# Optimization experiments

Measured on AMD Instinct MI355X. Metric: run time of the kernel, lower is better.

The kernel has to match this reference:

```python
import jax, jax.numpy as jnp
import numpy as np

ROWS = 1048576
DIM = 64
N_CHUNKS = 32
B = 32768


def setup_inputs() -> dict:
    key = jax.random.key(0)
    k_t, k_w, k_i0, k_i1 = jax.random.split(key, 4)
    bound = DIM ** (-0.5)
    table = jax.random.uniform(k_t, (ROWS, DIM), jnp.float32, -bound, bound)
    weights = jax.random.uniform(k_w, (ROWS * DIM, 1), jnp.float32, -1.0, 1.0)
    # Precomputed PolyHash outputs (fixed non-learned universal hashes)
    idx0 = jax.random.randint(k_i0, (B, N_CHUNKS), 0, ROWS, dtype=jnp.int64 if jax.config.jax_enable_x64 else jnp.int32)
    idx1 = jax.random.randint(k_i1, (B, N_CHUNKS), 0, ROWS * DIM, dtype=jnp.int64 if jax.config.jax_enable_x64 else jnp.int32)
    return {"table": table, "weights": weights, "idx0": idx0, "idx1": idx1}


def reference(table, weights, idx0, idx1):
    # vecs: [B, n_chunks, dim]; w: [B, n_chunks, 1]
    vecs = table[idx0]
    w = weights[idx1]
    return jnp.mean(vecs * w, axis=1)  # [B, dim]
```

## Files before the change

### kernel.cpp

```cpp
#include <hip/hip_runtime.h>

#define N_B 32768
#define N_CHUNKS 32
#define DIM 64

__global__ __launch_bounds__(256) void WeightedHashEmbedding_kernel(
    const float* __restrict__ table,
    const float* __restrict__ weights,
    const int*   __restrict__ idx0,
    const int*   __restrict__ idx1,
    float*       __restrict__ out)
{
    const int tid  = threadIdx.x;
    const int b    = blockIdx.x * 16 + (tid >> 4);
    const int quad = tid & 15;

    const int4* p0 = (const int4*)(idx0 + b * N_CHUNKS);
    const int4* p1 = (const int4*)(idx1 + b * N_CHUNKS);

    float4 acc = make_float4(0.f, 0.f, 0.f, 0.f);

    #pragma unroll 2
    for (int g = 0; g < N_CHUNKS / 4; ++g) {
        const int4 r0 = p0[g];
        const int4 r1 = p1[g];

        const float w0 = weights[r1.x];
        const float w1 = weights[r1.y];
        const float w2 = weights[r1.z];
        const float w3 = weights[r1.w];

        const float4 v0 = ((const float4*)(table + (size_t)r0.x * DIM))[quad];
        const float4 v1 = ((const float4*)(table + (size_t)r0.y * DIM))[quad];
        const float4 v2 = ((const float4*)(table + (size_t)r0.z * DIM))[quad];
        const float4 v3 = ((const float4*)(table + (size_t)r0.w * DIM))[quad];

        acc.x += v0.x * w0; acc.y += v0.y * w0; acc.z += v0.z * w0; acc.w += v0.w * w0;
        acc.x += v1.x * w1; acc.y += v1.y * w1; acc.z += v1.z * w1; acc.w += v1.w * w1;
        acc.x += v2.x * w2; acc.y += v2.y * w2; acc.z += v2.z * w2; acc.w += v2.w * w2;
        acc.x += v3.x * w3; acc.y += v3.y * w3; acc.z += v3.z * w3; acc.w += v3.w * w3;
    }

    const float inv = 1.0f / (float)N_CHUNKS;
    float4 r;
    r.x = acc.x * inv; r.y = acc.y * inv; r.z = acc.z * inv; r.w = acc.w * inv;
    ((float4*)(out + (size_t)b * DIM))[quad] = r;
}

extern "C" void kernel_launch(void* const* d_in, const int* in_sizes, int n_in,
                              void* d_out, int out_size, void* d_ws, size_t ws_size,
                              hipStream_t stream) {
    const float* table   = (const float*)d_in[0];
    const float* weights = (const float*)d_in[1];
    const int*   idx0    = (const int*)d_in[2];
    const int*   idx1    = (const int*)d_in[3];
    float*       out     = (float*)d_out;

    const int rows_per_block = 16;
    const int grid = N_B / rows_per_block;

    WeightedHashEmbedding_kernel<<<grid, 256, 0, stream>>>(table, weights, idx0, idx1, out);
}
```

Before: 473.4 us.

## Map one wavefront per batch row with lane-broadcast indices and weights

Each 64-lane wavefront now handles one batch row, with each lane owning one output dimension. The 32 indices and the 32 gathered weights are loaded once per wave, one per lane, and broadcast with readlane instead of being re-read by every thread. All 32 table-row loads are issued up front before any accumulation, which exposes more memory-level parallelism. The trade-offs are scalar 4-byte loads per lane instead of float4 loads, and higher register use to hold the 32 values in flight.

```diff
diff --git a/kernel.cpp b/kernel.cpp
--- a/kernel.cpp
+++ b/kernel.cpp
@@ -11,40 +11,30 @@
     const int*   __restrict__ idx1,
     float*       __restrict__ out)
 {
-    const int tid  = threadIdx.x;
-    const int b    = blockIdx.x * 16 + (tid >> 4);
-    const int quad = tid & 15;
+    const int lane = threadIdx.x & 63;
+    const int wid  = threadIdx.x >> 6;
+    const int b    = blockIdx.x * 4 + wid;
 
-    const int4* p0 = (const int4*)(idx0 + b * N_CHUNKS);
-    const int4* p1 = (const int4*)(idx1 + b * N_CHUNKS);
+    const int c  = lane & 31;
+    const int i0 = idx0[b * N_CHUNKS + c];
+    const int i1 = idx1[b * N_CHUNKS + c];
+    const float wv = weights[i1];
 
-    float4 acc = make_float4(0.f, 0.f, 0.f, 0.f);
-
-    #pragma unroll 2
-    for (int g = 0; g < N_CHUNKS / 4; ++g) {
-        const int4 r0 = p0[g];
-        const int4 r1 = p1[g];
-
-        const float w0 = weights[r1.x];
-        const float w1 = weights[r1.y];
-        const float w2 = weights[r1.z];
-        const float w3 = weights[r1.w];
-
-        const float4 v0 = ((const float4*)(table + (size_t)r0.x * DIM))[quad];
-        const float4 v1 = ((const float4*)(table + (size_t)r0.y * DIM))[quad];
-        const float4 v2 = ((const float4*)(table + (size_t)r0.z * DIM))[quad];
-        const float4 v3 = ((const float4*)(table + (size_t)r0.w * DIM))[quad];
-
-        acc.x += v0.x * w0; acc.y += v0.y * w0; acc.z += v0.z * w0; acc.w += v0.w * w0;
-        acc.x += v1.x * w1; acc.y += v1.y * w1; acc.z += v1.z * w1; acc.w += v1.w * w1;
-        acc.x += v2.x * w2; acc.y += v2.y * w2; acc.z += v2.z * w2; acc.w += v2.w * w2;
-        acc.x += v3.x * w3; acc.y += v3.y * w3; acc.z += v3.z * w3; acc.w += v3.w * w3;
+    float v[N_CHUNKS];
+    #pragma unroll
+    for (int cc = 0; cc < N_CHUNKS; ++cc) {
+        const int row = __builtin_amdgcn_readlane(i0, cc);
+        v[cc] = table[(size_t)row * DIM + lane];
     }
 
-    const float inv = 1.0f / (float)N_CHUNKS;
-    float4 r;
-    r.x = acc.x * inv; r.y = acc.y * inv; r.z = acc.z * inv; r.w = acc.w * inv;
-    ((float4*)(out + (size_t)b * DIM))[quad] = r;
+    float acc = 0.f;
+    #pragma unroll
+    for (int cc = 0; cc < N_CHUNKS; ++cc) {
+        const float w = __uint_as_float(__builtin_amdgcn_readlane(__float_as_uint(wv), cc));
+        acc += v[cc] * w;
+    }
+
+    out[(size_t)b * DIM + lane] = acc * (1.0f / (float)N_CHUNKS);
 }
 
 extern "C" void kernel_launch(void* const* d_in, const int* in_sizes, int n_in,
@@ -56,8 +46,7 @@
     const int*   idx1    = (const int*)d_in[3];
     float*       out     = (float*)d_out;
 
-    const int rows_per_block = 16;
+    const int rows_per_block = 4;
     const int grid = N_B / rows_per_block;
-
     WeightedHashEmbedding_kernel<<<grid, 256, 0, stream>>>(table, weights, idx0, idx1, out);
 }
```

Measured after the change: 471.8 us. Within noise of the previous version (-0.3%).
